# Kernel optimization log

Hardware: AMD Instinct MI355X
Metric: run time of the kernel (lower is better)

Reference implementation:

```python
import jax, jax.numpy as jnp
import numpy as np

B, N, H, R = 128, 512, 256, 3
VIRTUAL_DECAY = 0.7


def _build_tree():
    # Deterministic random recursive tree: parent[i] ~ U[0, i)
    rng = np.random.default_rng(0)
    parent = np.zeros(N, np.int64)
    for i in range(1, N):
        parent[i] = rng.integers(0, i)
    depth = np.zeros(N, np.int64)
    for i in range(1, N):
        depth[i] = depth[parent[i]] + 1
    rel_edge = rng.integers(0, R, N)          # relation type of edge (parent -> i)
    virtual = rng.random(N) < 0.1
    children = [[] for _ in range(N)]
    for i in range(1, N):
        children[parent[i]].append(i)
    # Group internal nodes by depth (deepest first == valid post-order batching),
    # pad ragged child lists per level.
    levels = []
    for d in range(int(depth.max()), -1, -1):
        nodes = [n for n in range(N) if depth[n] == d and len(children[n]) > 0]
        if not nodes:
            continue
        cmax = max(len(children[n]) for n in nodes)
        M = len(nodes)
        cidx = np.zeros((M, cmax), np.int64)
        cmask = np.zeros((M, cmax), np.float32)
        crel = np.zeros((M, cmax), np.int64)
        cvirt = np.zeros((M, cmax), bool)
        for m, n in enumerate(nodes):
            ch = children[n]
            k = len(ch)
            cidx[m, :k] = ch
            cmask[m, :k] = 1.0
            crel[m, :k] = rel_edge[ch]
            cvirt[m, :k] = virtual[ch]
        levels.append((jnp.array(nodes), jnp.array(cidx), jnp.array(cmask),
                       jnp.array(crel), jnp.array(cvirt)))
    return levels

LEVELS = _build_tree()


def _forward(node_features, W_enc, b_enc, rel_emb, W_i, b_i, W_o, b_o, W_u, b_u,
             W_f, b_f, w_attn, b_attn):
    h = node_features @ W_enc + b_enc            # (B, N, H) node_encoder
    c = jnp.zeros_like(h)
    for node_ids, cidx, cmask, crel, cvirt in LEVELS:
        x = h[:, node_ids]                       # (B, M, H) input_vec (== encoded feats)
        ch_h = h[:, cidx]                        # (B, M, C, H)
        ch_c = c[:, cidx]
        # virtual-node decay + padding mask
        decay = jnp.where(cvirt, VIRTUAL_DECAY, 1.0).astype(h.dtype) * cmask  # (M, C)
        ch_h = ch_h * decay[None, :, :, None]
        ch_c = ch_c * decay[None, :, :, None]
        # relation-aware attention over children
        re = rel_emb[crel]                       # (M, C, H)
        scores = jnp.einsum('bmch,h->bmc', re[None] + ch_h, w_attn) + b_attn[0]
        scores = jnp.where(cmask[None] > 0, scores, -1e9)
        attw = jax.nn.softmax(scores, axis=-1)   # (B, M, C)
        h_sum = jnp.einsum('bmc,bmch->bmh', attw, ch_h)
        # per-relation forget transform (note: original applies NO sigmoid here)
        f = jnp.zeros_like(ch_h)
        for r in range(R):
            fr = jnp.einsum('bmch,hk->bmck', ch_h, W_f[r]) + b_f[r]
            f = f + fr * (crel == r).astype(h.dtype)[None, :, :, None]
        c_sum = jnp.sum(f * ch_c, axis=2)        # (B, M, H); padded ch_c is 0
        comb = jnp.concatenate([x, h_sum], axis=-1)  # (B, M, 2H)
        i_g = jax.nn.sigmoid(comb @ W_i + b_i)
        o_g = jax.nn.sigmoid(comb @ W_o + b_o)
        u_g = jnp.tanh(comb @ W_u + b_u)
        c_new = i_g * u_g + c_sum
        h_new = o_g * jnp.tanh(c_new)
        h = h.at[:, node_ids].set(h_new)
        c = c.at[:, node_ids].set(c_new)
    return h[:, 0]                               # pooling == 'root' (root = 0)


def setup_inputs() -> dict:
    key = jax.random.key(0)
    ks = jax.random.split(key, 8)
    s = 0.05
    f32 = jnp.float32
    return {
        'node_features': jax.random.normal(ks[0], (B, N, H), f32),
        'W_enc': jax.random.normal(ks[1], (H, H), f32) * s,
        'b_enc': jnp.full((H,), 0.1, f32),
        'rel_emb': jax.random.normal(ks[2], (R, H), f32) * s,
        'W_i': jax.random.normal(ks[3], (2 * H, H), f32) * s,
        'b_i': jnp.full((H,), 0.1, f32),
        'W_o': jax.random.normal(ks[4], (2 * H, H), f32) * s,
        'b_o': jnp.full((H,), 0.1, f32),
        'W_u': jax.random.normal(ks[5], (2 * H, H), f32) * s,
        'b_u': jnp.full((H,), 0.1, f32),
        'W_f': jax.random.normal(ks[6], (R, H, H), f32) * s,
        'b_f': jnp.full((R, H), 0.1, f32),
        'w_attn': jax.random.normal(ks[7], (H,), f32) * s,
        'b_attn': jnp.full((1,), 0.1, f32),
    }


def reference(node_features, W_enc, b_enc, rel_emb, W_i, b_i, W_o, b_o, W_u, b_u,
              W_f, b_f, w_attn, b_attn):
    return _forward(node_features, W_enc, b_enc, rel_emb, W_i, b_i, W_o, b_o,
                    W_u, b_u, W_f, b_f, w_attn, b_attn)
```

## Files before the change

### kernel.cpp

```cpp
#include <hip/hip_runtime.h>
#include <stdint.h>
#include <string.h>
#include <math.h>

#define NB 128
#define NN 512
#define NH 256
#define NR 3
#define TH_TINY 8

typedef __attribute__((ext_vector_type(8))) short bh8;
typedef __attribute__((ext_vector_type(4))) float f32x4;

struct Pcg {
  __uint128_t state, inc;
  bool has32; uint32_t buf32;
};

static const __uint128_t PCG_MULT =
    (((__uint128_t)2549297995355413924ULL) << 64) | 4865540595714422341ULL;

static inline uint64_t pcg_next64(Pcg& s) {
  s.state = s.state * PCG_MULT + s.inc;
  uint64_t hi = (uint64_t)(s.state >> 64), lo = (uint64_t)s.state;
  uint64_t x = hi ^ lo;
  unsigned rot = (unsigned)(s.state >> 122) & 63u;
  return (x >> rot) | (x << ((64u - rot) & 63u));
}
static inline uint32_t pcg_next32(Pcg& s) {
  if (s.has32) { s.has32 = false; return s.buf32; }
  uint64_t n = pcg_next64(s);
  s.has32 = true; s.buf32 = (uint32_t)(n >> 32);
  return (uint32_t)n;
}
static inline uint64_t pcg_bounded(Pcg& s, uint64_t high) {
  uint64_t rng = high - 1;
  if (rng == 0) return 0;
  uint32_t rng_excl = (uint32_t)rng + 1u;
  uint64_t m = (uint64_t)pcg_next32(s) * (uint64_t)rng_excl;
  uint32_t leftover = (uint32_t)m;
  if (leftover < rng_excl) {
    uint32_t threshold = (uint32_t)((0xFFFFFFFFu - (uint32_t)rng) % rng_excl);
    while (leftover < threshold) {
      m = (uint64_t)pcg_next32(s) * (uint64_t)rng_excl;
      leftover = (uint32_t)m;
    }
  }
  return m >> 32;
}
static inline double pcg_double(Pcg& s) {
  return (double)(pcg_next64(s) >> 11) * (1.0 / 9007199254740992.0);
}

static void pcg_seed0(Pcg& s) {
  uint32_t pool[4];
  uint32_t hc = 0x43b0d7e5u;
  auto hashmix = [&hc](uint32_t v) -> uint32_t {
    v ^= hc; hc *= 0x931e8875u; v *= hc; v ^= v >> 16; return v;
  };
  auto mix = [](uint32_t x, uint32_t y) -> uint32_t {
    uint32_t r = 0xca01f9ddu * x - 0x4973f715u * y; r ^= r >> 16; return r;
  };
  for (int i = 0; i < 4; i++) pool[i] = hashmix(0u);
  for (int src = 0; src < 4; src++)
    for (int dst = 0; dst < 4; dst++)
      if (src != dst) pool[dst] = mix(pool[dst], hashmix(pool[src]));
  uint32_t gs[8]; uint32_t hb = 0x8b51f9ddu;
  for (int i = 0; i < 8; i++) {
    uint32_t dv = pool[i & 3];
    dv ^= hb; hb *= 0x58f38dedu; dv *= hb; dv ^= dv >> 16;
    gs[i] = dv;
  }
  uint64_t w0 = (uint64_t)gs[0] | ((uint64_t)gs[1] << 32);
  uint64_t w1 = (uint64_t)gs[2] | ((uint64_t)gs[3] << 32);
  uint64_t w2 = (uint64_t)gs[4] | ((uint64_t)gs[5] << 32);
  uint64_t w3 = (uint64_t)gs[6] | ((uint64_t)gs[7] << 32);
  __uint128_t initstate = (((__uint128_t)w0) << 64) | w1;
  __uint128_t initseq   = (((__uint128_t)w2) << 64) | w3;
  s.state = 0;
  s.inc = (initseq << 1) | 1;
  s.state = s.state * PCG_MULT + s.inc;
  s.state += initstate;
  s.state = s.state * PCG_MULT + s.inc;
  s.has32 = false; s.buf32 = 0;
}

struct TreeMeta {
  int nodes[512];
  int cstart[512];
  int ccount[512];
  int echild[512];
  int erel[512];
  float edecay[512];
  int cechild[512];
  int cerel[512];
  float cedec[512];
  int cens[513];
};
struct HostTree {
  TreeMeta meta;
  int n_levels;
  int level_off[520];
  int level_M[520];
};

static void build_tree_host(HostTree& T) {
  Pcg st; pcg_seed0(st);
  int parent[NN], depth[NN], rel[NN];
  unsigned char virt[NN];
  parent[0] = 0; depth[0] = 0;
  for (int i = 1; i < NN; i++) parent[i] = (int)pcg_bounded(st, (uint64_t)i);
  for (int i = 1; i < NN; i++) depth[i] = depth[parent[i]] + 1;
  for (int i = 0; i < NN; i++) rel[i] = (int)pcg_bounded(st, (uint64_t)NR);
  for (int i = 0; i < NN; i++) virt[i] = (pcg_double(st) < 0.1) ? 1 : 0;

  int childcnt[NN]; memset(childcnt, 0, sizeof(childcnt));
  for (int i = 1; i < NN; i++) childcnt[parent[i]]++;
  int maxd = 0;
  for (int i = 0; i < NN; i++) if (depth[i] > maxd) maxd = depth[i];

  int ni = 0, ne = 0, nec = 0;
  T.n_levels = 0;
  for (int d = maxd; d >= 0; d--) {
    int mstart = ni;
    for (int n = 0; n < NN; n++) {
      if (depth[n] == d && childcnt[n] > 0) {
        T.meta.nodes[ni] = n;
        T.meta.cstart[ni] = ne;
        T.meta.ccount[ni] = childcnt[n];
        T.meta.cens[ni] = nec;
        for (int i2 = 1; i2 < NN; i2++) {
          if (parent[i2] == n) {
            T.meta.echild[ne] = i2;
            T.meta.erel[ne] = rel[i2];
            T.meta.edecay[ne] = virt[i2] ? 0.7f : 1.0f;
            ne++;
            if (childcnt[i2] > 0) {
              T.meta.cechild[nec] = i2;
              T.meta.cerel[nec] = rel[i2];
              T.meta.cedec[nec] = virt[i2] ? 0.7f : 1.0f;
              nec++;
            }
          }
        }
        ni++;
      }
    }
    if (ni > mstart) {
      T.level_off[T.n_levels] = mstart;
      T.level_M[T.n_levels] = ni - mstart;
      T.n_levels++;
    }
  }
  T.meta.cens[ni] = nec;
}

__device__ __forceinline__ uint16_t f2bf(float f) {
  uint32_t u = __float_as_uint(f);
  return (uint16_t)((u + 0x7fffu + ((u >> 16) & 1u)) >> 16);
}
__device__ __forceinline__ float bf2f(uint16_t b) {
  return __uint_as_float(((uint32_t)b) << 16);
}
__device__ __forceinline__ float sigm(float x) {
  return 1.f / (1.f + expf(-x));
}

__device__ __forceinline__ void stage_bf16(uint16_t* __restrict__ sm,
    const uint16_t* __restrict__ src, int stride, int rows) {
  const int chunks = rows << 3;
  for (int cch = threadIdx.x; cch < chunks; cch += 256) {
    const int row = cch >> 3, k = (cch & 7) << 3;
    uint4 v = *(const uint4*)(src + (size_t)row * stride + k);
    *(uint4*)(sm + (((row << 6) + k) ^ ((row & 7) << 3))) = v;
  }
}
__device__ __forceinline__ void stage_f32(uint16_t* __restrict__ sm,
    const float* __restrict__ src, int stride, int rows) {
  const int chunks = rows << 3;
  for (int cch = threadIdx.x; cch < chunks; cch += 256) {
    const int row = cch >> 3, k = (cch & 7) << 3;
    const float* p = src + (size_t)row * stride + k;
    float4 a = *(const float4*)p, b = *(const float4*)(p + 4);
    uint4 w;
    w.x = (uint32_t)f2bf(a.x) | ((uint32_t)f2bf(a.y) << 16);
    w.y = (uint32_t)f2bf(a.z) | ((uint32_t)f2bf(a.w) << 16);
    w.z = (uint32_t)f2bf(b.x) | ((uint32_t)f2bf(b.y) << 16);
    w.w = (uint32_t)f2bf(b.z) | ((uint32_t)f2bf(b.w) << 16);
    *(uint4*)(sm + (((row << 6) + k) ^ ((row & 7) << 3))) = w;
  }
}
__device__ __forceinline__ bh8 fld(const uint16_t* __restrict__ sm, int row, int k) {
  return *(const bh8*)(sm + (((row << 6) + k) ^ ((row & 7) << 3)));
}

__global__ __launch_bounds__(256) void k_prep(const float* __restrict__ We,
    const float* __restrict__ Wf, const float* __restrict__ Wi,
    const float* __restrict__ Wo, const float* __restrict__ Wu,
    uint16_t* __restrict__ WeT, uint16_t* __restrict__ WfT,
    uint16_t* __restrict__ WgT) {
  const int i = blockIdx.x * 256 + threadIdx.x;
  if (i < 65536) {
    const int n = i >> 8, k = i & 255;
    WeT[i] = f2bf(We[k * 256 + n]);
  }
  const int i2 = i - 65536;
  if (i2 >= 0 && i2 < 196608) {
    const int r = i2 >> 16, rem = i2 & 65535, n = rem >> 8, k = rem & 255;
    WfT[i2] = f2bf(Wf[r * 65536 + k * 256 + n]);
  }
  const int i3 = i - 262144;
  if (i3 >= 0 && i3 < 393216) {
    const int g = i3 >> 17, rem = i3 & 131071, n = rem >> 9, k = rem & 511;
    const float* S = (g == 0) ? Wi : (g == 1) ? Wo : Wu;
    WgT[i3] = f2bf(S[k * 256 + n]);
  }
}

__global__ __launch_bounds__(256) void k_enc(const float* __restrict__ nf,
    const uint16_t* __restrict__ WeT, const float* __restrict__ b_enc,
    uint16_t* __restrict__ h_bf) {
  __shared__ __align__(16) uint16_t smA[128 * 64];
  __shared__ __align__(16) uint16_t smB[128 * 64];
  const int bm = blockIdx.x * 128, bn = blockIdx.y * 128;
  const int tid = threadIdx.x, wid = tid >> 6, lane = tid & 63;
  const int wr = wid >> 1, wc2 = wid & 1, lr = lane & 15, lk = (lane >> 4) << 3;
  f32x4 acc[4][4] = {};
  for (int k0 = 0; k0 < 256; k0 += 64) {
    __syncthreads();
    stage_f32(smA, nf + (size_t)bm * NH + k0, NH, 128);
    stage_bf16(smB, WeT + (size_t)bn * 256 + k0, 256, 128);
    __syncthreads();
#pragma unroll
    for (int ks = 0; ks < 2; ks++) {
      bh8 af[4], bfr[4];
#pragma unroll
      for (int i = 0; i < 4; i++) af[i] = fld(smA, wr * 64 + i * 16 + lr, ks * 32 + lk);
#pragma unroll
      for (int j = 0; j < 4; j++) bfr[j] = fld(smB, wc2 * 64 + j * 16 + lr, ks * 32 + lk);
#pragma unroll
      for (int i = 0; i < 4; i++)
#pragma unroll
        for (int j = 0; j < 4; j++)
          acc[i][j] = __builtin_amdgcn_mfma_f32_16x16x32_bf16(af[i], bfr[j], acc[i][j], 0, 0, 0);
    }
  }
#pragma unroll
  for (int i = 0; i < 4; i++) {
#pragma unroll
    for (int j = 0; j < 4; j++) {
      const int col = bn + wc2 * 64 + j * 16 + (lane & 15);
      const float be = b_enc[col];
#pragma unroll
      for (int r = 0; r < 4; r++) {
        const int row = bm + wr * 64 + i * 16 + (lane >> 4) * 4 + r;
        h_bf[(size_t)row * NH + col] = f2bf(acc[i][j][r] + be);
      }
    }
  }
}

__global__ __launch_bounds__(256) void k_lvl(
    uint16_t* h_bf, float* c,
    const uint16_t* __restrict__ WfT, const uint16_t* __restrict__ WgT,
    const float* __restrict__ b_f, const float* __restrict__ b_i,
    const float* __restrict__ b_o, const float* __restrict__ b_u,
    const float* __restrict__ rel_emb, const float* __restrict__ w_attn,
    const float* __restrict__ b_attn, float* __restrict__ out,
    const TreeMeta* __restrict__ tm, int nb) {
  __shared__ float sc[64 * 65];
  __shared__ float swa[256];
  __shared__ float sRE[3];
  __shared__ int chl[64]; __shared__ int rll[64]; __shared__ float dcl[64];
  __shared__ __align__(16) uint16_t hsum[4 * 4096];

  const int bx = blockIdx.x, mloc = bx >> 1, b0 = (bx & 1) * 64;
  const int cslice = blockIdx.y * 64;
  const int gi = nb + mloc;
  const int nd = tm->nodes[gi], cs = tm->cstart[gi], cc = tm->ccount[gi];
  const int ce0 = tm->cens[gi], nic = tm->cens[gi + 1] - ce0;
  const int tid = threadIdx.x, wid = tid >> 6, lane = tid & 63;
  const int lr2 = lane & 15, hi4 = (lane >> 4), lk = hi4 << 3;
  const int colw = cslice + wid * 16 + lr2;

  if (tid < cc) {
    chl[tid] = tm->echild[cs + tid];
    rll[tid] = tm->erel[cs + tid];
    dcl[tid] = tm->edecay[cs + tid];
  }
  swa[tid] = w_attn[tid];
  if (wid < 3) {
    float p = 0.f;
#pragma unroll
    for (int i = 0; i < 4; i++) p += rel_emb[wid * NH + lane + 64 * i] * w_attn[lane + 64 * i];
#pragma unroll
    for (int off = 32; off; off >>= 1) p += __shfl_down(p, off);
    if (lane == 0) sRE[wid] = p;
  }
  __syncthreads();

  const int sb = tid >> 2, sq = tid & 3;
  const float ba = b_attn[0];
  for (int e = 0; e < cc; e++) {
    const uint16_t* hp = h_bf + ((size_t)(b0 + sb) * NN + chl[e]) * NH + sq * 64;
    float s = 0.f;
#pragma unroll
    for (int v = 0; v < 8; v++) {
      uint4 pk = *(const uint4*)(hp + v * 8);
      const uint16_t* pe = (const uint16_t*)&pk;
#pragma unroll
      for (int q = 0; q < 8; q++) s = fmaf(bf2f(pe[q]), swa[sq * 64 + v * 8 + q], s);
    }
    s += __shfl_xor(s, 1); s += __shfl_xor(s, 2);
    if (sq == 0) sc[sb * 65 + e] = sRE[rll[e]] + dcl[e] * s + ba;
  }
  __syncthreads();
  if (tid < 64) {
    float mx = -1e30f;
    for (int e = 0; e < cc; e++) mx = fmaxf(mx, sc[tid * 65 + e]);
    float ss = 0.f;
    for (int e = 0; e < cc; e++) ss += expf(sc[tid * 65 + e] - mx);
    const float inv = 1.0f / ss;
    for (int e = 0; e < cc; e++) sc[tid * 65 + e] = expf(sc[tid * 65 + e] - mx) * inv * dcl[e];
  }
  __syncthreads();

  {
    float hs[64];
#pragma unroll
    for (int v = 0; v < 64; v++) hs[v] = 0.f;
    for (int e = 0; e < cc; e++) {
      const float w = sc[sb * 65 + e];
      const uint16_t* hp = h_bf + ((size_t)(b0 + sb) * NN + chl[e]) * NH + sq * 64;
#pragma unroll
      for (int v = 0; v < 8; v++) {
        uint4 pk = *(const uint4*)(hp + v * 8);
        const uint16_t* pe = (const uint16_t*)&pk;
#pragma unroll
        for (int q = 0; q < 8; q++) hs[v * 8 + q] = fmaf(bf2f(pe[q]), w, hs[v * 8 + q]);
      }
    }
    uint16_t* sub = hsum + sq * 4096;
#pragma unroll
    for (int v = 0; v < 32; v++) {
      uint32_t pk = (uint32_t)f2bf(hs[2 * v]) | ((uint32_t)f2bf(hs[2 * v + 1]) << 16);
      const int elem = ((sb << 6) + 2 * v) ^ ((sb & 7) << 3);
      *(uint32_t*)(sub + elem) = pk;
    }
  }

  f32x4 csum[4] = {};
  for (int e = 0; e < nic; e++) {
    const int ch = tm->cechild[ce0 + e];
    const int rel = tm->cerel[ce0 + e];
    const float dec = tm->cedec[ce0 + e];
    const uint16_t* Wr = WfT + (size_t)rel * 65536 + (size_t)colw * 256;
    f32x4 facc[4] = {};
#pragma unroll
    for (int k0 = 0; k0 < 8; k0++) {
      const int kk = k0 * 32 + lk;
      bh8 af[4];
#pragma unroll
      for (int i = 0; i < 4; i++)
        af[i] = *(const bh8*)(h_bf + ((size_t)(b0 + i * 16 + lr2) * NN + ch) * NH + kk);
      const bh8 bq = *(const bh8*)(Wr + kk);
#pragma unroll
      for (int i = 0; i < 4; i++)
        facc[i] = __builtin_amdgcn_mfma_f32_16x16x32_bf16(af[i], bq, facc[i], 0, 0, 0);
    }
    const float bfv = b_f[rel * NH + colw];
#pragma unroll
    for (int i = 0; i < 4; i++) {
#pragma unroll
      for (int r = 0; r < 4; r++) {
        const int brow = b0 + i * 16 + hi4 * 4 + r;
        const float cch = c[((size_t)brow * NN + ch) * NH + colw];
        csum[i][r] += (dec * facc[i][r] + bfv) * (dec * cch);
      }
    }
  }
  __syncthreads();

  f32x4 ga[3][4] = {};
#pragma unroll
  for (int k32 = 0; k32 < 16; k32++) {
    const int kk = k32 * 32 + lk;
    bh8 af[4], bq[3];
    if (k32 < 8) {
#pragma unroll
      for (int i = 0; i < 4; i++)
        af[i] = *(const bh8*)(h_bf + ((size_t)(b0 + i * 16 + lr2) * NN + nd) * NH + kk);
    } else {
      const int kx = k32 - 8;
#pragma unroll
      for (int i = 0; i < 4; i++)
        af[i] = fld(hsum + (kx >> 1) * 4096, i * 16 + lr2, (kx & 1) * 32 + lk);
    }
#pragma unroll
    for (int g = 0; g < 3; g++)
      bq[g] = *(const bh8*)(WgT + ((size_t)g << 17) + (size_t)colw * 512 + kk);
#pragma unroll
    for (int g = 0; g < 3; g++)
#pragma unroll
      for (int i = 0; i < 4; i++)
        ga[g][i] = __builtin_amdgcn_mfma_f32_16x16x32_bf16(af[i], bq[g], ga[g][i], 0, 0, 0);
  }

  const float bi_ = b_i[colw], bo_ = b_o[colw], bu_ = b_u[colw];
#pragma unroll
  for (int i = 0; i < 4; i++) {
#pragma unroll
    for (int r = 0; r < 4; r++) {
      const int brow = b0 + i * 16 + hi4 * 4 + r;
      const size_t idx = ((size_t)brow * NN + nd) * NH + colw;
      const float ig = sigm(ga[0][i][r] + bi_);
      const float og = sigm(ga[1][i][r] + bo_);
      const float ug = tanhf(ga[2][i][r] + bu_);
      const float cn = fmaf(ig, ug, csum[i][r]);
      c[idx] = cn;
      const float hn = og * tanhf(cn);
      h_bf[idx] = f2bf(hn);
      if (nd == 0) out[(size_t)brow * NH + colw] = hn;
    }
  }
}

__global__ __launch_bounds__(256) void k_tiny(
    uint16_t* h_bf, float* c,
    const uint16_t* __restrict__ WfT, const uint16_t* __restrict__ WgT,
    const float* __restrict__ b_f, const float* __restrict__ b_i,
    const float* __restrict__ b_o, const float* __restrict__ b_u,
    const float* __restrict__ rel_emb, const float* __restrict__ w_attn,
    const float* __restrict__ b_attn, float* __restrict__ out,
    const TreeMeta* __restrict__ tm, int nb) {
  __shared__ float sc[64 * 65];
  __shared__ float swa[256];
  __shared__ float sRE[3];
  __shared__ int chl[64]; __shared__ int rll[64]; __shared__ float dcl[64];
  __shared__ __align__(16) uint16_t hsum[4 * 4096];

  const int c0 = blockIdx.x * 16;
  const int mloc = blockIdx.y >> 1, b0 = (blockIdx.y & 1) * 64;
  const int gi = nb + mloc;
  const int nd = tm->nodes[gi], cs = tm->cstart[gi], cc = tm->ccount[gi];
  const int ce0 = tm->cens[gi], nic = tm->cens[gi + 1] - ce0;
  const int tid = threadIdx.x, wid = tid >> 6, lane = tid & 63;
  const int lb = lane & 15, lq = lane >> 4;
  const int colw = c0 + lb;
  const int wrow = b0 + wid * 16;

  if (tid < cc) {
    chl[tid] = tm->echild[cs + tid];
    rll[tid] = tm->erel[cs + tid];
    dcl[tid] = tm->edecay[cs + tid];
  }
  swa[tid] = w_attn[tid];
  if (wid < 3) {
    float p = 0.f;
#pragma unroll
    for (int i = 0; i < 4; i++) p += rel_emb[wid * NH + lane + 64 * i] * w_attn[lane + 64 * i];
#pragma unroll
    for (int off = 32; off; off >>= 1) p += __shfl_down(p, off);
    if (lane == 0) sRE[wid] = p;
  }
  __syncthreads();

  const int sb = tid >> 2, sq = tid & 3;
  const float ba = b_attn[0];
  for (int e = 0; e < cc; e++) {
    const uint16_t* hp = h_bf + ((size_t)(b0 + sb) * NN + chl[e]) * NH + sq * 64;
    float s = 0.f;
#pragma unroll
    for (int v = 0; v < 8; v++) {
      uint4 pk = *(const uint4*)(hp + v * 8);
      const uint16_t* pe = (const uint16_t*)&pk;
#pragma unroll
      for (int q = 0; q < 8; q++) s = fmaf(bf2f(pe[q]), swa[sq * 64 + v * 8 + q], s);
    }
    s += __shfl_xor(s, 1); s += __shfl_xor(s, 2);
    if (sq == 0) sc[sb * 65 + e] = sRE[rll[e]] + dcl[e] * s + ba;
  }
  __syncthreads();
  if (tid < 64) {
    float mx = -1e30f;
    for (int e = 0; e < cc; e++) mx = fmaxf(mx, sc[tid * 65 + e]);
    float ss = 0.f;
    for (int e = 0; e < cc; e++) ss += expf(sc[tid * 65 + e] - mx);
    const float inv = 1.0f / ss;
    for (int e = 0; e < cc; e++) sc[tid * 65 + e] = expf(sc[tid * 65 + e] - mx) * inv * dcl[e];
  }
  __syncthreads();

  {
    float hs[64];
#pragma unroll
    for (int v = 0; v < 64; v++) hs[v] = 0.f;
    for (int e = 0; e < cc; e++) {
      const float w = sc[sb * 65 + e];
      const uint16_t* hp = h_bf + ((size_t)(b0 + sb) * NN + chl[e]) * NH + sq * 64;
#pragma unroll
      for (int v = 0; v < 8; v++) {
        uint4 pk = *(const uint4*)(hp + v * 8);
        const uint16_t* pe = (const uint16_t*)&pk;
#pragma unroll
        for (int q = 0; q < 8; q++) hs[v * 8 + q] = fmaf(bf2f(pe[q]), w, hs[v * 8 + q]);
      }
    }
    uint16_t* sub = hsum + sq * 4096;
#pragma unroll
    for (int v = 0; v < 32; v++) {
      uint32_t pk = (uint32_t)f2bf(hs[2 * v]) | ((uint32_t)f2bf(hs[2 * v + 1]) << 16);
      const int elem = ((sb << 6) + 2 * v) ^ ((sb & 7) << 3);
      *(uint32_t*)(sub + elem) = pk;
    }
  }

  f32x4 csum = {};
  for (int e = 0; e < nic; e++) {
    const int ch = tm->cechild[ce0 + e];
    const int rel = tm->cerel[ce0 + e];
    const float dec = tm->cedec[ce0 + e];
    const uint16_t* Wr = WfT + (size_t)rel * 65536 + (size_t)colw * 256;
    f32x4 facc = {};
#pragma unroll
    for (int k0 = 0; k0 < 8; k0++) {
      const int kk = k0 * 32 + lq * 8;
      const bh8 af = *(const bh8*)(h_bf + ((size_t)(wrow + lb) * NN + ch) * NH + kk);
      const bh8 bq = *(const bh8*)(Wr + kk);
      facc = __builtin_amdgcn_mfma_f32_16x16x32_bf16(af, bq, facc, 0, 0, 0);
    }
    const float bfv = b_f[rel * NH + colw];
#pragma unroll
    for (int r = 0; r < 4; r++) {
      const int brow = wrow + lq * 4 + r;
      const float cch = c[((size_t)brow * NN + ch) * NH + colw];
      csum[r] += (dec * facc[r] + bfv) * (dec * cch);
    }
  }
  __syncthreads();

  f32x4 ga[3] = {};
#pragma unroll
  for (int k32 = 0; k32 < 16; k32++) {
    const int kk = k32 * 32 + lq * 8;
    bh8 af;
    if (k32 < 8) {
      af = *(const bh8*)(h_bf + ((size_t)(wrow + lb) * NN + nd) * NH + kk);
    } else {
      const int kx = k32 - 8;
      af = fld(hsum + (kx >> 1) * 4096, wid * 16 + lb, (kx & 1) * 32 + lq * 8);
    }
#pragma unroll
    for (int g = 0; g < 3; g++) {
      const bh8 bq = *(const bh8*)(WgT + ((size_t)g << 17) + (size_t)colw * 512 + kk);
      ga[g] = __builtin_amdgcn_mfma_f32_16x16x32_bf16(af, bq, ga[g], 0, 0, 0);
    }
  }

  const float bi_ = b_i[colw], bo_ = b_o[colw], bu_ = b_u[colw];
#pragma unroll
  for (int r = 0; r < 4; r++) {
    const int brow = wrow + lq * 4 + r;
    const size_t idx = ((size_t)brow * NN + nd) * NH + colw;
    const float ig = sigm(ga[0][r] + bi_);
    const float og = sigm(ga[1][r] + bo_);
    const float ug = tanhf(ga[2][r] + bu_);
    const float cn = fmaf(ig, ug, csum[r]);
    c[idx] = cn;
    const float hn = og * tanhf(cn);
    h_bf[idx] = f2bf(hn);
    if (nd == 0) out[(size_t)brow * NH + colw] = hn;
  }
}

extern "C" void kernel_launch(void* const* d_in, const int* in_sizes, int n_in,
                              void* d_out, int out_size, void* d_ws, size_t ws_size,
                              hipStream_t stream) {
  (void)in_sizes; (void)n_in; (void)out_size; (void)ws_size;
  const float* nf      = (const float*)d_in[0];
  const float* W_enc   = (const float*)d_in[1];
  const float* b_enc   = (const float*)d_in[2];
  const float* rel_emb = (const float*)d_in[3];
  const float* W_i     = (const float*)d_in[4];
  const float* b_i     = (const float*)d_in[5];
  const float* W_o     = (const float*)d_in[6];
  const float* b_o     = (const float*)d_in[7];
  const float* W_u     = (const float*)d_in[8];
  const float* b_u     = (const float*)d_in[9];
  const float* W_f     = (const float*)d_in[10];
  const float* b_f     = (const float*)d_in[11];
  const float* w_attn  = (const float*)d_in[12];
  const float* b_attn  = (const float*)d_in[13];
  float* out = (float*)d_out;

  static HostTree T;
  build_tree_host(T);

  char* ws = (char*)d_ws;
  const size_t OFF_HBF = 32768;
  const size_t SZ_HBF  = (size_t)NB * NN * NH * 2;
  const size_t OFF_WET = OFF_HBF + SZ_HBF;
  const size_t OFF_WFT = OFF_WET + 131072;
  const size_t OFF_WGT = OFF_WFT + 393216;
  const size_t OFF_C   = OFF_WGT + 786432;

  TreeMeta* dm = (TreeMeta*)ws;
  uint16_t* h_bf = (uint16_t*)(ws + OFF_HBF);
  uint16_t* WeT = (uint16_t*)(ws + OFF_WET);
  uint16_t* WfT = (uint16_t*)(ws + OFF_WFT);
  uint16_t* WgT = (uint16_t*)(ws + OFF_WGT);
  float* c = (float*)(ws + OFF_C);

  hipMemcpyAsync(dm, &T.meta, sizeof(TreeMeta), hipMemcpyHostToDevice, stream);

  k_prep<<<2560, 256, 0, stream>>>(W_enc, W_f, W_i, W_o, W_u, WeT, WfT, WgT);
  k_enc<<<dim3((NB * NN) / 128, 2), 256, 0, stream>>>(nf, WeT, b_enc, h_bf);

  for (int l = 0; l < T.n_levels; l++) {
    const int Mfull = T.level_M[l];
    if (Mfull >= TH_TINY) {
      for (int c0 = 0; c0 < Mfull; c0 += 128) {
        const int Mc = (Mfull - c0) < 128 ? (Mfull - c0) : 128;
        k_lvl<<<dim3(2 * Mc, 4), 256, 0, stream>>>(h_bf, c, WfT, WgT,
            b_f, b_i, b_o, b_u, rel_emb, w_attn, b_attn, out, dm,
            T.level_off[l] + c0);
      }
    } else {
      k_tiny<<<dim3(16, 2 * Mfull), 256, 0, stream>>>(h_bf, c, WfT, WgT,
          b_f, b_i, b_o, b_u, rel_emb, w_attn, b_attn, out, dm,
          T.level_off[l]);
    }
  }
}
```

Measured before the change: 682.0 us.

## Precompute per-node attention partial scores and keep separate encoded-input buffer

The attention score for each child is no longer recomputed by a full 256-wide dot product in every level kernel. Instead, 16 partial dot products with w_attn are stored per (batch, node), first by a new k_sv0 pass and then by each level kernel's epilogue when it writes the new h. A separate copy of the encoded features (x_enc) is kept so the gate GEMM reads the original input rather than the overwritten h. The change also double-buffers the child-row loads in the weighted sum, adds unroll 2 on the child-c loop, and raises the threshold below which the tiny-level kernel is used. In exchange it adds an extra workspace buffer and extra memory traffic for the partial scores and x_enc.

```diff
diff --git a/kernel.cpp b/kernel.cpp
--- a/kernel.cpp
+++ b/kernel.cpp
@@ -7,7 +7,7 @@
 #define NN 512
 #define NH 256
 #define NR 3
-#define TH_TINY 8
+#define TH_TINY 24
 
 typedef __attribute__((ext_vector_type(8))) short bh8;
 typedef __attribute__((ext_vector_type(4))) float f32x4;
@@ -194,6 +194,16 @@
   return *(const bh8*)(sm + (((row << 6) + k) ^ ((row & 7) << 3)));
 }
 
+#define LDROW(BUF, CH) do { \
+    const uint4* p_ = (const uint4*)(hbase + (size_t)(CH) * NH); \
+    BUF[0]=p_[0]; BUF[1]=p_[1]; BUF[2]=p_[2]; BUF[3]=p_[3]; \
+    BUF[4]=p_[4]; BUF[5]=p_[5]; BUF[6]=p_[6]; BUF[7]=p_[7]; } while (0)
+#define ACCROW(BUF, W) do { const float w_ = (W); \
+    _Pragma("unroll") for (int v_ = 0; v_ < 8; v_++) { \
+      const uint16_t* pe_ = (const uint16_t*)&BUF[v_]; \
+      _Pragma("unroll") for (int q_ = 0; q_ < 8; q_++) \
+        hs[v_*8+q_] = fmaf(bf2f(pe_[q_]), w_, hs[v_*8+q_]); } } while (0)
+
 __global__ __launch_bounds__(256) void k_prep(const float* __restrict__ We,
     const float* __restrict__ Wf, const float* __restrict__ Wi,
     const float* __restrict__ Wo, const float* __restrict__ Wu,
@@ -219,7 +229,7 @@
 
 __global__ __launch_bounds__(256) void k_enc(const float* __restrict__ nf,
     const uint16_t* __restrict__ WeT, const float* __restrict__ b_enc,
-    uint16_t* __restrict__ h_bf) {
+    uint16_t* __restrict__ h_bf, uint16_t* __restrict__ x_enc) {
   __shared__ __align__(16) uint16_t smA[128 * 64];
   __shared__ __align__(16) uint16_t smB[128 * 64];
   const int bm = blockIdx.x * 128, bn = blockIdx.y * 128;
@@ -254,14 +264,34 @@
 #pragma unroll
       for (int r = 0; r < 4; r++) {
         const int row = bm + wr * 64 + i * 16 + (lane >> 4) * 4 + r;
-        h_bf[(size_t)row * NH + col] = f2bf(acc[i][j][r] + be);
+        const uint16_t hv = f2bf(acc[i][j][r] + be);
+        h_bf[(size_t)row * NH + col] = hv;
+        x_enc[(size_t)row * NH + col] = hv;
       }
     }
   }
 }
 
+__global__ __launch_bounds__(256) void k_sv0(const uint16_t* __restrict__ h_bf,
+    const float* __restrict__ w_attn, float* __restrict__ svp) {
+  const int idx = blockIdx.x * 256 + threadIdx.x;
+  const int g = idx & 15;
+  const size_t row = (size_t)(idx >> 4);
+  const uint16_t* hp = h_bf + row * NH + g * 16;
+  uint4 p0 = *(const uint4*)hp, p1 = *(const uint4*)(hp + 8);
+  const uint16_t* e0 = (const uint16_t*)&p0;
+  const uint16_t* e1 = (const uint16_t*)&p1;
+  float s = 0.f;
+#pragma unroll
+  for (int u = 0; u < 8; u++) s = fmaf(bf2f(e0[u]), w_attn[g * 16 + u], s);
+#pragma unroll
+  for (int u = 0; u < 8; u++) s = fmaf(bf2f(e1[u]), w_attn[g * 16 + 8 + u], s);
+  svp[idx] = s;
+}
+
 __global__ __launch_bounds__(256) void k_lvl(
-    uint16_t* h_bf, float* c,
+    uint16_t* h_bf, float* c, float* __restrict__ svp,
+    const uint16_t* __restrict__ x_enc,
     const uint16_t* __restrict__ WfT, const uint16_t* __restrict__ WgT,
     const float* __restrict__ b_f, const float* __restrict__ b_i,
     const float* __restrict__ b_o, const float* __restrict__ b_u,
@@ -299,23 +329,16 @@
   }
   __syncthreads();
 
-  const int sb = tid >> 2, sq = tid & 3;
   const float ba = b_attn[0];
-  for (int e = 0; e < cc; e++) {
-    const uint16_t* hp = h_bf + ((size_t)(b0 + sb) * NN + chl[e]) * NH + sq * 64;
-    float s = 0.f;
-#pragma unroll
-    for (int v = 0; v < 8; v++) {
-      uint4 pk = *(const uint4*)(hp + v * 8);
-      const uint16_t* pe = (const uint16_t*)&pk;
-#pragma unroll
-      for (int q = 0; q < 8; q++) s = fmaf(bf2f(pe[q]), swa[sq * 64 + v * 8 + q], s);
-    }
-    s += __shfl_xor(s, 1); s += __shfl_xor(s, 2);
-    if (sq == 0) sc[sb * 65 + e] = sRE[rll[e]] + dcl[e] * s + ba;
-  }
-  __syncthreads();
   if (tid < 64) {
+    const float* svpb = svp + (size_t)(b0 + tid) * NN * 16;
+    for (int e = 0; e < cc; e++) {
+      const float4* p = (const float4*)(svpb + chl[e] * 16);
+      float4 a = p[0], b2 = p[1], c2 = p[2], d2 = p[3];
+      float s = ((a.x + a.y) + (a.z + a.w)) + ((b2.x + b2.y) + (b2.z + b2.w)) +
+                ((c2.x + c2.y) + (c2.z + c2.w)) + ((d2.x + d2.y) + (d2.z + d2.w));
+      sc[tid * 65 + e] = sRE[rll[e]] + dcl[e] * s + ba;
+    }
     float mx = -1e30f;
     for (int e = 0; e < cc; e++) mx = fmaxf(mx, sc[tid * 65 + e]);
     float ss = 0.f;
@@ -325,21 +348,22 @@
   }
   __syncthreads();
 
+  const int sb = tid >> 2, sq = tid & 3;
   {
     float hs[64];
 #pragma unroll
     for (int v = 0; v < 64; v++) hs[v] = 0.f;
-    for (int e = 0; e < cc; e++) {
-      const float w = sc[sb * 65 + e];
-      const uint16_t* hp = h_bf + ((size_t)(b0 + sb) * NN + chl[e]) * NH + sq * 64;
-#pragma unroll
-      for (int v = 0; v < 8; v++) {
-        uint4 pk = *(const uint4*)(hp + v * 8);
-        const uint16_t* pe = (const uint16_t*)&pk;
-#pragma unroll
-        for (int q = 0; q < 8; q++) hs[v * 8 + q] = fmaf(bf2f(pe[q]), w, hs[v * 8 + q]);
-      }
-    }
+    const uint16_t* hbase = h_bf + (size_t)(b0 + sb) * NN * NH + sq * 64;
+    uint4 bufA[8], bufB[8];
+    LDROW(bufA, chl[0]);
+    int e = 0;
+    for (; e + 2 <= cc; e += 2) {
+      LDROW(bufB, chl[e + 1]);
+      ACCROW(bufA, sc[sb * 65 + e]);
+      if (e + 2 < cc) LDROW(bufA, chl[e + 2]);
+      ACCROW(bufB, sc[sb * 65 + e + 1]);
+    }
+    if (e < cc) ACCROW(bufA, sc[sb * 65 + e]);
     uint16_t* sub = hsum + sq * 4096;
 #pragma unroll
     for (int v = 0; v < 32; v++) {
@@ -350,6 +374,7 @@
   }
 
   f32x4 csum[4] = {};
+#pragma unroll 2
   for (int e = 0; e < nic; e++) {
     const int ch = tm->cechild[ce0 + e];
     const int rel = tm->cerel[ce0 + e];
@@ -389,7 +414,7 @@
     if (k32 < 8) {
 #pragma unroll
       for (int i = 0; i < 4; i++)
-        af[i] = *(const bh8*)(h_bf + ((size_t)(b0 + i * 16 + lr2) * NN + nd) * NH + kk);
+        af[i] = *(const bh8*)(x_enc + ((size_t)(b0 + i * 16 + lr2) * NN + nd) * NH + kk);
     } else {
       const int kx = k32 - 8;
 #pragma unroll
@@ -407,6 +432,7 @@
   }
 
   const float bi_ = b_i[colw], bo_ = b_o[colw], bu_ = b_u[colw];
+  const float wac = swa[colw];
 #pragma unroll
   for (int i = 0; i < 4; i++) {
 #pragma unroll
@@ -421,12 +447,17 @@
       const float hn = og * tanhf(cn);
       h_bf[idx] = f2bf(hn);
       if (nd == 0) out[(size_t)brow * NH + colw] = hn;
+      float pv = hn * wac;
+      pv += __shfl_xor(pv, 1); pv += __shfl_xor(pv, 2);
+      pv += __shfl_xor(pv, 4); pv += __shfl_xor(pv, 8);
+      if (lr2 == 0) svp[((size_t)brow * NN + nd) * 16 + (cslice >> 4) + wid] = pv;
     }
   }
 }
 
 __global__ __launch_bounds__(256) void k_tiny(
-    uint16_t* h_bf, float* c,
+    uint16_t* h_bf, float* c, float* __restrict__ svp,
+    const uint16_t* __restrict__ x_enc,
     const uint16_t* __restrict__ WfT, const uint16_t* __restrict__ WgT,
     const float* __restrict__ b_f, const float* __restrict__ b_i,
     const float* __restrict__ b_o, const float* __restrict__ b_u,
@@ -465,23 +496,16 @@
   }
   __syncthreads();
 
-  const int sb = tid >> 2, sq = tid & 3;
   const float ba = b_attn[0];
-  for (int e = 0; e < cc; e++) {
-    const uint16_t* hp = h_bf + ((size_t)(b0 + sb) * NN + chl[e]) * NH + sq * 64;
-    float s = 0.f;
-#pragma unroll
-    for (int v = 0; v < 8; v++) {
-      uint4 pk = *(const uint4*)(hp + v * 8);
-      const uint16_t* pe = (const uint16_t*)&pk;
-#pragma unroll
-      for (int q = 0; q < 8; q++) s = fmaf(bf2f(pe[q]), swa[sq * 64 + v * 8 + q], s);
-    }
-    s += __shfl_xor(s, 1); s += __shfl_xor(s, 2);
-    if (sq == 0) sc[sb * 65 + e] = sRE[rll[e]] + dcl[e] * s + ba;
-  }
-  __syncthreads();
   if (tid < 64) {
+    const float* svpb = svp + (size_t)(b0 + tid) * NN * 16;
+    for (int e = 0; e < cc; e++) {
+      const float4* p = (const float4*)(svpb + chl[e] * 16);
+      float4 a = p[0], b2 = p[1], c2 = p[2], d2 = p[3];
+      float s = ((a.x + a.y) + (a.z + a.w)) + ((b2.x + b2.y) + (b2.z + b2.w)) +
+                ((c2.x + c2.y) + (c2.z + c2.w)) + ((d2.x + d2.y) + (d2.z + d2.w));
+      sc[tid * 65 + e] = sRE[rll[e]] + dcl[e] * s + ba;
+    }
     float mx = -1e30f;
     for (int e = 0; e < cc; e++) mx = fmaxf(mx, sc[tid * 65 + e]);
     float ss = 0.f;
@@ -491,21 +515,22 @@
   }
   __syncthreads();
 
+  const int sb = tid >> 2, sq = tid & 3;
   {
     float hs[64];
 #pragma unroll
     for (int v = 0; v < 64; v++) hs[v] = 0.f;
-    for (int e = 0; e < cc; e++) {
-      const float w = sc[sb * 65 + e];
-      const uint16_t* hp = h_bf + ((size_t)(b0 + sb) * NN + chl[e]) * NH + sq * 64;
-#pragma unroll
-      for (int v = 0; v < 8; v++) {
-        uint4 pk = *(const uint4*)(hp + v * 8);
-        const uint16_t* pe = (const uint16_t*)&pk;
-#pragma unroll
-        for (int q = 0; q < 8; q++) hs[v * 8 + q] = fmaf(bf2f(pe[q]), w, hs[v * 8 + q]);
-      }
-    }
+    const uint16_t* hbase = h_bf + (size_t)(b0 + sb) * NN * NH + sq * 64;
+    uint4 bufA[8], bufB[8];
+    LDROW(bufA, chl[0]);
+    int e = 0;
+    for (; e + 2 <= cc; e += 2) {
+      LDROW(bufB, chl[e + 1]);
+      ACCROW(bufA, sc[sb * 65 + e]);
+      if (e + 2 < cc) LDROW(bufA, chl[e + 2]);
+      ACCROW(bufB, sc[sb * 65 + e + 1]);
+    }
+    if (e < cc) ACCROW(bufA, sc[sb * 65 + e]);
     uint16_t* sub = hsum + sq * 4096;
 #pragma unroll
     for (int v = 0; v < 32; v++) {
@@ -516,6 +541,7 @@
   }
 
   f32x4 csum = {};
+#pragma unroll 2
   for (int e = 0; e < nic; e++) {
     const int ch = tm->cechild[ce0 + e];
     const int rel = tm->cerel[ce0 + e];
@@ -545,7 +571,7 @@
     const int kk = k32 * 32 + lq * 8;
     bh8 af;
     if (k32 < 8) {
-      af = *(const bh8*)(h_bf + ((size_t)(wrow + lb) * NN + nd) * NH + kk);
+      af = *(const bh8*)(x_enc + ((size_t)(wrow + lb) * NN + nd) * NH + kk);
     } else {
       const int kx = k32 - 8;
       af = fld(hsum + (kx >> 1) * 4096, wid * 16 + lb, (kx & 1) * 32 + lq * 8);
@@ -558,6 +584,7 @@
   }
 
   const float bi_ = b_i[colw], bo_ = b_o[colw], bu_ = b_u[colw];
+  const float wac = swa[colw];
 #pragma unroll
   for (int r = 0; r < 4; r++) {
     const int brow = wrow + lq * 4 + r;
@@ -570,6 +597,10 @@
     const float hn = og * tanhf(cn);
     h_bf[idx] = f2bf(hn);
     if (nd == 0) out[(size_t)brow * NH + colw] = hn;
+    float pv = hn * wac;
+    pv += __shfl_xor(pv, 1); pv += __shfl_xor(pv, 2);
+    pv += __shfl_xor(pv, 4); pv += __shfl_xor(pv, 8);
+    if (lb == 0) svp[((size_t)brow * NN + nd) * 16 + (c0 >> 4)] = pv;
   }
 }
 
@@ -599,34 +630,40 @@
   char* ws = (char*)d_ws;
   const size_t OFF_HBF = 32768;
   const size_t SZ_HBF  = (size_t)NB * NN * NH * 2;
-  const size_t OFF_WET = OFF_HBF + SZ_HBF;
+  const size_t OFF_XE  = OFF_HBF + SZ_HBF;
+  const size_t OFF_WET = OFF_XE + SZ_HBF;
   const size_t OFF_WFT = OFF_WET + 131072;
   const size_t OFF_WGT = OFF_WFT + 393216;
   const size_t OFF_C   = OFF_WGT + 786432;
+  const size_t SZ_C    = (size_t)NB * NN * NH * 4;
+  const size_t OFF_SVP = OFF_C + SZ_C;
 
   TreeMeta* dm = (TreeMeta*)ws;
   uint16_t* h_bf = (uint16_t*)(ws + OFF_HBF);
+  uint16_t* x_enc = (uint16_t*)(ws + OFF_XE);
   uint16_t* WeT = (uint16_t*)(ws + OFF_WET);
   uint16_t* WfT = (uint16_t*)(ws + OFF_WFT);
   uint16_t* WgT = (uint16_t*)(ws + OFF_WGT);
   float* c = (float*)(ws + OFF_C);
+  float* svp = (float*)(ws + OFF_SVP);
 
   hipMemcpyAsync(dm, &T.meta, sizeof(TreeMeta), hipMemcpyHostToDevice, stream);
 
   k_prep<<<2560, 256, 0, stream>>>(W_enc, W_f, W_i, W_o, W_u, WeT, WfT, WgT);
-  k_enc<<<dim3((NB * NN) / 128, 2), 256, 0, stream>>>(nf, WeT, b_enc, h_bf);
+  k_enc<<<dim3((NB * NN) / 128, 2), 256, 0, stream>>>(nf, WeT, b_enc, h_bf, x_enc);
+  k_sv0<<<dim3((NB * NN * 16) / 256), 256, 0, stream>>>(h_bf, w_attn, svp);
 
   for (int l = 0; l < T.n_levels; l++) {
     const int Mfull = T.level_M[l];
     if (Mfull >= TH_TINY) {
       for (int c0 = 0; c0 < Mfull; c0 += 128) {
         const int Mc = (Mfull - c0) < 128 ? (Mfull - c0) : 128;
-        k_lvl<<<dim3(2 * Mc, 4), 256, 0, stream>>>(h_bf, c, WfT, WgT,
+        k_lvl<<<dim3(2 * Mc, 4), 256, 0, stream>>>(h_bf, c, svp, x_enc, WfT, WgT,
             b_f, b_i, b_o, b_u, rel_emb, w_attn, b_attn, out, dm,
             T.level_off[l] + c0);
       }
     } else {
-      k_tiny<<<dim3(16, 2 * Mfull), 256, 0, stream>>>(h_bf, c, WfT, WgT,
+      k_tiny<<<dim3(16, 2 * Mfull), 256, 0, stream>>>(h_bf, c, svp, x_enc, WfT, WgT,
           b_f, b_i, b_o, b_u, rel_emb, w_attn, b_attn, out, dm,
           T.level_off[l]);
     }
```

Result: faster. 612.9 us (-10.1%).
